# Performance work log

Hardware: AMD Instinct MI355X
Metric: run time of the kernel (lower is better)

Reference implementation:

```python
import jax, jax.numpy as jnp
import numpy as np
from jax import lax

T, H, K, V, O = 8192, 2048, 512, 512, 2048


def setup_inputs() -> dict:
    key = jax.random.key(0)
    ks = jax.random.split(key, 11)
    s_h = 1.0 / np.sqrt(H)
    s_v = 1.0 / np.sqrt(V)
    return {
        "hidden_state": jax.random.normal(ks[0], (T, H), jnp.float32),
        "Wq": jax.random.normal(ks[1], (H, K), jnp.float32) * s_h,
        "bq": jax.random.normal(ks[2], (K,), jnp.float32) * 0.02,
        "Wk": jax.random.normal(ks[3], (H, K), jnp.float32) * s_h,
        "bk": jax.random.normal(ks[4], (K,), jnp.float32) * 0.02,
        "Wv": jax.random.normal(ks[5], (H, V), jnp.float32) * s_h,
        "bv": jax.random.normal(ks[6], (V,), jnp.float32) * 0.02,
        "Wg": jax.random.normal(ks[7], (H, K), jnp.float32) * s_h,
        "bg": jax.random.normal(ks[8], (K,), jnp.float32) * 0.02,
        "Wo": jax.random.normal(ks[9], (V, O), jnp.float32) * s_v,
        "bo": jax.random.normal(ks[10], (O,), jnp.float32) * 0.02,
    }


def reference(hidden_state, Wq, bq, Wk, bk, Wv, bv, Wg, bg, Wo, bo):
    # Batched projections (torch Linear: x @ W^T + b; here W stored as [in,out])
    q = hidden_state @ Wq + bq                    # [T, K]
    k = jax.nn.sigmoid(hidden_state @ Wk + bk)    # [T, K]
    g = jax.nn.sigmoid(hidden_state @ Wg + bg)    # [T, K]
    v = hidden_state @ Wv + bv                    # [T, V]

    def step(state, qkvg):
        qi, ki, vi, gi = qkvg
        # state: [K, V]; gated decay per key-dim row, then outer-product write
        state = state * gi[:, None] + ki[:, None] * vi[None, :]
        out_i = qi @ state  # == state.T @ qi -> [V]
        return state, out_i

    init = jnp.zeros((K, V), hidden_state.dtype)
    final_state, outs = lax.scan(step, init, (q, k, v, g))  # outs: [T, V]
    output = outs @ Wo + bo                                  # [T, O]
    return output, final_state
```

## Files before the change

kernel.cpp:

```cpp
#include <hip/hip_runtime.h>

#define T_LEN 8192
#define H_DIM 2048
#define K_DIM 512
#define V_DIM 512
#define O_DIM 2048
#define CHUNK 64
#define NCHUNK 128

typedef short bf16x8 __attribute__((ext_vector_type(8)));
typedef float f32x4 __attribute__((ext_vector_type(4)));

typedef const __attribute__((address_space(1))) void* gptr1_t;
typedef __attribute__((address_space(3))) void* lptr3_t;

__device__ __forceinline__ float b2f(unsigned short u) {
    unsigned int i = ((unsigned int)u) << 16;
    float f;
    __builtin_memcpy(&f, &i, 4);
    return f;
}
__device__ __forceinline__ unsigned short f2b(float f) {
    unsigned int i;
    __builtin_memcpy(&i, &f, 4);
    unsigned int r = (i + 0x7FFFu + ((i >> 16) & 1u)) >> 16;
    return (unsigned short)r;
}
__device__ __forceinline__ float fw(float v) {
    return fminf(fmaxf(v, -1e30f), 1e30f);
}

#define BARX() asm volatile("s_barrier" ::: "memory")
#define ORDER() asm volatile("" ::: "memory")

#define GLDS(gp, dstByte)                                                      \
    __builtin_amdgcn_global_load_lds((gptr1_t)(const void*)(gp),               \
                                     (lptr3_t)(void*)((char*)lds + (dstByte)), \
                                     16, 0, 0)
#define STAGE2(p0, p1, dstBase)                                                \
    do {                                                                       \
        GLDS(p0, (dstBase) + tid * 16);                                        \
        GLDS(p1, (dstBase) + 8192 + tid * 16);                                 \
    } while (0)

__global__ __launch_bounds__(64) void probe_k(int* __restrict__ flag) {
    __shared__ unsigned short As[16 * 32];
    __shared__ unsigned short Bs[16 * 32];
    int tid = threadIdx.x;
    for (int idx = tid; idx < 512; idx += 64) {
        int r = idx >> 5, c = idx & 31;
        float av = (c == 0) ? (float)(r + 1) : (c == 1 ? 1.0f : 0.0f);
        float bv = (c == 0) ? 1.0f : (c == 1 ? (float)(1024 * (r + 1)) : 0.0f);
        As[r * 32 + c] = f2b(av);
        Bs[r * 32 + c] = f2b(bv);
    }
    __syncthreads();
    int ln15 = tid & 15, q4 = (tid & 63) >> 4;
    bf16x8 a = *(const bf16x8*)(As + ln15 * 32 + q4 * 8);
    bf16x8 b = *(const bf16x8*)(Bs + ln15 * 32 + q4 * 8);
    f32x4 acc = {0.f, 0.f, 0.f, 0.f};
    acc = __builtin_amdgcn_mfma_f32_16x16x32_bf16(a, b, acc, 0, 0, 0);
    bool h0 = true, h1 = true;
#pragma unroll
    for (int i = 0; i < 4; i++) {
        float e0 = (float)((q4 * 4 + i + 1) + 1024 * (ln15 + 1));
        float e1 = (float)((ln15 + 1) + 1024 * (q4 * 4 + i + 1));
        h0 = h0 && (acc[i] == e0);
        h1 = h1 && (acc[i] == e1);
    }
    unsigned long long b0 = __ballot(h0 ? 1 : 0);
    unsigned long long b1 = __ballot(h1 ? 1 : 0);
    if (tid == 0) *flag = (b0 == ~0ull) ? 0 : ((b1 == ~0ull) ? 1 : 0);
}

__global__ __launch_bounds__(256) void prep_k(const float* __restrict__ hs,
                                              unsigned short* __restrict__ hsb,
                                              const float* __restrict__ Wq,
                                              const float* __restrict__ Wk,
                                              const float* __restrict__ Wg,
                                              const float* __restrict__ Wv,
                                              const float* __restrict__ Wo,
                                              unsigned short* __restrict__ WT,
                                              unsigned short* __restrict__ WoT) {
    __shared__ unsigned short tile[32][33];
    long bid = blockIdx.x;
    int tid = threadIdx.x;
    if (bid < 8192) {
        long i = (bid * 256 + tid) * 8;
        unsigned int wd[4];
#pragma unroll
        for (int u = 0; u < 4; u++) {
            unsigned short lo = f2b(hs[i + 2 * u]);
            unsigned short hi = f2b(hs[i + 2 * u + 1]);
            wd[u] = (unsigned int)lo | ((unsigned int)hi << 16);
        }
        uint4 pk; pk.x = wd[0]; pk.y = wd[1]; pk.z = wd[2]; pk.w = wd[3];
        *(uint4*)(hsb + i) = pk;
        return;
    }
    int t = (int)(bid - 8192);
    int mat = t >> 10, tl = t & 1023;
    const float* in; unsigned short* outp; int R, C, br, bc;
    if (mat < 4) {
        in = mat == 0 ? Wq : mat == 1 ? Wk : mat == 2 ? Wg : Wv;
        outp = WT + (long)mat * 512 * H_DIM;
        R = H_DIM; C = 512; br = tl >> 4; bc = tl & 15;
    } else {
        in = Wo; outp = WoT; R = V_DIM; C = O_DIM; br = tl & 15; bc = tl >> 4;
    }
    int tc = tid & 31, tr = tid >> 5;
#pragma unroll
    for (int i = 0; i < 4; i++) {
        int r = tr + 8 * i;
        long idx = (long)(br * 32 + r) * C + bc * 32 + tc;
        tile[r][tc] = f2b(in[idx]);
    }
    __syncthreads();
#pragma unroll
    for (int i = 0; i < 4; i++) {
        int r = tr + 8 * i;
        outp[(long)(bc * 32 + r) * R + br * 32 + tc] = tile[tc][r];
    }
}

__global__ __launch_bounds__(512, 2) void proj_gemm256_k(const unsigned short* __restrict__ A,
                                                         const unsigned short* __restrict__ WT,
                                                         const float* __restrict__ bq,
                                                         const float* __restrict__ bk,
                                                         const float* __restrict__ bg,
                                                         const float* __restrict__ bv,
                                                         unsigned short* __restrict__ qb,
                                                         unsigned short* __restrict__ kb,
                                                         float* __restrict__ gb,
                                                         unsigned short* __restrict__ vT,
                                                         const int* __restrict__ flagp) {
    __shared__ short lds[65536];
    int fl = *flagp;
    int tid = threadIdx.x;
    int lane = tid & 63;
    int ln15 = lane & 15, q4 = lane >> 4;
    int w = tid >> 6;
    int wm = w >> 2, wn = w & 3;
    long m0 = (long)blockIdx.x * 256, n0 = (long)blockIdx.y * 256;

    unsigned slot = ((unsigned)(q4 * 16)) ^ ((unsigned)((ln15 & 7) << 4));
    unsigned aoff0 = (unsigned)(wm * 8192 + ln15 * 128) + slot;
    unsigned boff0 = 65536u + (unsigned)(wn * 4096 + ln15 * 128) + slot;

    int idx0 = tid, idx1 = 512 + tid;
    int r0_ = idx0 >> 3, r1_ = idx1 >> 3;
    int c80 = (idx0 & 7) ^ (r0_ & 7);
    int c81 = (idx1 & 7) ^ (r1_ & 7);
    int trA0 = ((r0_ >> 6) & 1) * 128 + (r0_ & 63);
    int trA1 = ((r1_ >> 6) & 1) * 128 + (r1_ & 63);
    int tcB0 = ((r0_ >> 5) & 3) * 64 + (r0_ & 31);
    int tcB1 = ((r1_ >> 5) & 3) * 64 + (r1_ & 31);
    const unsigned short* pAlo0 = A + (m0 + trA0) * (long)H_DIM + c80 * 8;
    const unsigned short* pAlo1 = A + (m0 + trA1) * (long)H_DIM + c81 * 8;
    const unsigned short* pAhi0 = pAlo0 + 64 * H_DIM;
    const unsigned short* pAhi1 = pAlo1 + 64 * H_DIM;
    const unsigned short* pBlo0 = WT + (n0 + tcB0) * (long)H_DIM + c80 * 8;
    const unsigned short* pBlo1 = WT + (n0 + tcB1) * (long)H_DIM + c81 * 8;
    const unsigned short* pBhi0 = pBlo0 + 32 * H_DIM;
    const unsigned short* pBhi1 = pBlo1 + 32 * H_DIM;

    f32x4 acc[8][4] = {};

    STAGE2(pAlo0, pAlo1, 0);
    STAGE2(pBlo0, pBlo1, 65536);
    ORDER();
    STAGE2(pBhi0, pBhi1, 65536 + 16384);
    STAGE2(pAhi0, pAhi1, 16384);
    ORDER();
    pAlo0 += 64; pAlo1 += 64; pBlo0 += 64; pBlo1 += 64;
    STAGE2(pAlo0, pAlo1, 32768);
    STAGE2(pBlo0, pBlo1, 65536 + 32768);
    ORDER();
    pAlo0 += 64; pAlo1 += 64; pBlo0 += 64; pBlo1 += 64;
    pAhi0 += 64; pAhi1 += 64; pBhi0 += 64; pBhi1 += 64;
    asm volatile("s_waitcnt vmcnt(8)" ::: "memory");
    BARX();

    int cur = 0;
    const char* L = (const char*)lds;
    for (int kt = 0; kt < H_DIM; kt += 64, cur ^= 1) {
        int nxt = cur ^ 1;
        unsigned bufb = (unsigned)cur << 15;
        unsigned ab0 = aoff0 + bufb, ab1 = ab0 ^ 64u;
        unsigned bb0 = boff0 + bufb, bb1 = bb0 ^ 64u;
        bf16x8 af[4][2], blo[2][2], bhi[2][2];

#pragma unroll
        for (int i = 0; i < 4; i++) {
            af[i][0] = *(const bf16x8*)(L + ab0 + i * 2048);
            af[i][1] = *(const bf16x8*)(L + ab1 + i * 2048);
        }
#pragma unroll
        for (int j = 0; j < 2; j++) {
            blo[j][0] = *(const bf16x8*)(L + bb0 + j * 2048);
            blo[j][1] = *(const bf16x8*)(L + bb1 + j * 2048);
        }
        STAGE2(pBhi0, pBhi1, 65536 + nxt * 32768 + 16384);
        BARX();
        __builtin_amdgcn_s_setprio(1);
#pragma unroll
        for (int i = 0; i < 4; i++)
#pragma unroll
            for (int j = 0; j < 2; j++) {
                acc[i][j] = __builtin_amdgcn_mfma_f32_16x16x32_bf16(af[i][0], blo[j][0], acc[i][j], 0, 0, 0);
                acc[i][j] = __builtin_amdgcn_mfma_f32_16x16x32_bf16(af[i][1], blo[j][1], acc[i][j], 0, 0, 0);
            }
        __builtin_amdgcn_s_setprio(0);
        asm volatile("s_waitcnt vmcnt(8)" ::: "memory");
        BARX();

#pragma unroll
        for (int j = 0; j < 2; j++) {
            bhi[j][0] = *(const bf16x8*)(L + bb0 + 16384 + j * 2048);
            bhi[j][1] = *(const bf16x8*)(L + bb1 + 16384 + j * 2048);
        }
        STAGE2(pAhi0, pAhi1, nxt * 32768 + 16384);
        BARX();
        __builtin_amdgcn_s_setprio(1);
#pragma unroll
        for (int i = 0; i < 4; i++)
#pragma unroll
            for (int j = 0; j < 2; j++) {
                acc[i][2 + j] = __builtin_amdgcn_mfma_f32_16x16x32_bf16(af[i][0], bhi[j][0], acc[i][2 + j], 0, 0, 0);
                acc[i][2 + j] = __builtin_amdgcn_mfma_f32_16x16x32_bf16(af[i][1], bhi[j][1], acc[i][2 + j], 0, 0, 0);
            }
        __builtin_amdgcn_s_setprio(0);
        asm volatile("s_waitcnt vmcnt(8)" ::: "memory");
        BARX();

#pragma unroll
        for (int i = 0; i < 4; i++) {
            af[i][0] = *(const bf16x8*)(L + ab0 + 16384 + i * 2048);
            af[i][1] = *(const bf16x8*)(L + ab1 + 16384 + i * 2048);
        }
        STAGE2(pAlo0, pAlo1, cur * 32768);
        BARX();
        __builtin_amdgcn_s_setprio(1);
#pragma unroll
        for (int i = 0; i < 4; i++)
#pragma unroll
            for (int j = 0; j < 2; j++) {
                acc[4 + i][2 + j] = __builtin_amdgcn_mfma_f32_16x16x32_bf16(af[i][0], bhi[j][0], acc[4 + i][2 + j], 0, 0, 0);
                acc[4 + i][2 + j] = __builtin_amdgcn_mfma_f32_16x16x32_bf16(af[i][1], bhi[j][1], acc[4 + i][2 + j], 0, 0, 0);
            }
        __builtin_amdgcn_s_setprio(0);
        BARX();

        STAGE2(pBlo0, pBlo1, 65536 + cur * 32768);
        __builtin_amdgcn_s_setprio(1);
#pragma unroll
        for (int i = 0; i < 4; i++)
#pragma unroll
            for (int j = 0; j < 2; j++) {
                acc[4 + i][j] = __builtin_amdgcn_mfma_f32_16x16x32_bf16(af[i][0], blo[j][0], acc[4 + i][j], 0, 0, 0);
                acc[4 + i][j] = __builtin_amdgcn_mfma_f32_16x16x32_bf16(af[i][1], blo[j][1], acc[4 + i][j], 0, 0, 0);
            }
        __builtin_amdgcn_s_setprio(0);
        asm volatile("s_waitcnt vmcnt(8)" ::: "memory");
        BARX();

        pAlo0 += 64; pAlo1 += 64; pAhi0 += 64; pAhi1 += 64;
        pBlo0 += 64; pBlo1 += 64; pBhi0 += 64; pBhi1 += 64;
    }

    int seg = (int)(n0 >> 9);
    int nl0 = (int)(n0 & 511);
    const float* bias = seg == 0 ? bq : seg == 1 ? bk : seg == 2 ? bg : bv;

    if (seg == 3 && fl == 0) {
#pragma unroll
        for (int im = 0; im < 8; im++)
#pragma unroll
            for (int jn = 0; jn < 4; jn++) {
                int nl = nl0 + wn * 64 + (jn >> 1) * 32 + (jn & 1) * 16 + ln15;
                float bsv = bias[nl];
                long mb = m0 + wm * 128 + (im >> 2) * 64 + (im & 3) * 16 + q4 * 4;
                unsigned short h0 = f2b(fw(acc[im][jn][0] + bsv));
                unsigned short h1 = f2b(fw(acc[im][jn][1] + bsv));
                unsigned short h2 = f2b(fw(acc[im][jn][2] + bsv));
                unsigned short h3 = f2b(fw(acc[im][jn][3] + bsv));
                uint2 pk;
                pk.x = (unsigned int)h0 | ((unsigned int)h1 << 16);
                pk.y = (unsigned int)h2 | ((unsigned int)h3 << 16);
                *(uint2*)(vT + (long)nl * T_LEN + mb) = pk;
            }
    } else {
#pragma unroll
        for (int im = 0; im < 8; im++)
#pragma unroll
            for (int jn = 0; jn < 4; jn++)
#pragma unroll
                for (int ii = 0; ii < 4; ii++) {
                    int dm = fl ? ln15 : q4 * 4 + ii;
                    int dn = fl ? q4 * 4 + ii : ln15;
                    long m = m0 + wm * 128 + (im >> 2) * 64 + (im & 3) * 16 + dm;
                    int nl = nl0 + wn * 64 + (jn >> 1) * 32 + (jn & 1) * 16 + dn;
                    float v = fw(acc[im][jn][ii] + bias[nl]);
                    if (seg == 1 || seg == 2) v = 1.0f / (1.0f + __expf(-v));
                    if (seg == 0)
                        qb[m * K_DIM + nl] = f2b(v);
                    else if (seg == 1)
                        kb[m * K_DIM + nl] = f2b(v);
                    else if (seg == 2)
                        gb[m * K_DIM + nl] = v;
                    else
                        vT[(long)nl * T_LEN + m] = f2b(v);
                }
    }
}

__global__ __launch_bounds__(512, 2) void gemm256_k(const unsigned short* __restrict__ A,
                                                    const unsigned short* __restrict__ BT,
                                                    const float* __restrict__ bias,
                                                    float* __restrict__ out,
                                                    int N, int KT,
                                                    const int* __restrict__ flagp) {
    __shared__ short lds[65536];
    int fl = *flagp;
    int tid = threadIdx.x;
    int lane = tid & 63;
    int ln15 = lane & 15, q4 = lane >> 4;
    int w = tid >> 6;
    int wm = w >> 2, wn = w & 3;
    long m0 = (long)blockIdx.x * 256, n0 = (long)blockIdx.y * 256;

    unsigned slot = ((unsigned)(q4 * 16)) ^ ((unsigned)((ln15 & 7) << 4));
    unsigned aoff0 = (unsigned)(wm * 8192 + ln15 * 128) + slot;
    unsigned boff0 = 65536u + (unsigned)(wn * 4096 + ln15 * 128) + slot;

    int idx0 = tid, idx1 = 512 + tid;
    int r0_ = idx0 >> 3, r1_ = idx1 >> 3;
    int c80 = (idx0 & 7) ^ (r0_ & 7);
    int c81 = (idx1 & 7) ^ (r1_ & 7);
    int trA0 = ((r0_ >> 6) & 1) * 128 + (r0_ & 63);
    int trA1 = ((r1_ >> 6) & 1) * 128 + (r1_ & 63);
    int tcB0 = ((r0_ >> 5) & 3) * 64 + (r0_ & 31);
    int tcB1 = ((r1_ >> 5) & 3) * 64 + (r1_ & 31);
    const unsigned short* pAlo0 = A + (m0 + trA0) * (long)KT + c80 * 8;
    const unsigned short* pAlo1 = A + (m0 + trA1) * (long)KT + c81 * 8;
    const unsigned short* pAhi0 = pAlo0 + 64 * KT;
    const unsigned short* pAhi1 = pAlo1 + 64 * KT;
    const unsigned short* pBlo0 = BT + (n0 + tcB0) * (long)KT + c80 * 8;
    const unsigned short* pBlo1 = BT + (n0 + tcB1) * (long)KT + c81 * 8;
    const unsigned short* pBhi0 = pBlo0 + 32 * KT;
    const unsigned short* pBhi1 = pBlo1 + 32 * KT;

    f32x4 acc[8][4] = {};

    STAGE2(pAlo0, pAlo1, 0);
    STAGE2(pBlo0, pBlo1, 65536);
    ORDER();
    STAGE2(pBhi0, pBhi1, 65536 + 16384);
    STAGE2(pAhi0, pAhi1, 16384);
    ORDER();
    pAlo0 += 64; pAlo1 += 64; pBlo0 += 64; pBlo1 += 64;
    STAGE2(pAlo0, pAlo1, 32768);
    STAGE2(pBlo0, pBlo1, 65536 + 32768);
    ORDER();
    pAlo0 += 64; pAlo1 += 64; pBlo0 += 64; pBlo1 += 64;
    pAhi0 += 64; pAhi1 += 64; pBhi0 += 64; pBhi1 += 64;
    asm volatile("s_waitcnt vmcnt(8)" ::: "memory");
    BARX();

    int cur = 0;
    const char* L = (const char*)lds;
    for (int kt = 0; kt < KT; kt += 64, cur ^= 1) {
        int nxt = cur ^ 1;
        unsigned bufb = (unsigned)cur << 15;
        unsigned ab0 = aoff0 + bufb, ab1 = ab0 ^ 64u;
        unsigned bb0 = boff0 + bufb, bb1 = bb0 ^ 64u;
        bf16x8 af[4][2], blo[2][2], bhi[2][2];

#pragma unroll
        for (int i = 0; i < 4; i++) {
            af[i][0] = *(const bf16x8*)(L + ab0 + i * 2048);
            af[i][1] = *(const bf16x8*)(L + ab1 + i * 2048);
        }
#pragma unroll
        for (int j = 0; j < 2; j++) {
            blo[j][0] = *(const bf16x8*)(L + bb0 + j * 2048);
            blo[j][1] = *(const bf16x8*)(L + bb1 + j * 2048);
        }
        STAGE2(pBhi0, pBhi1, 65536 + nxt * 32768 + 16384);
        BARX();
        __builtin_amdgcn_s_setprio(1);
#pragma unroll
        for (int i = 0; i < 4; i++)
#pragma unroll
            for (int j = 0; j < 2; j++) {
                acc[i][j] = __builtin_amdgcn_mfma_f32_16x16x32_bf16(af[i][0], blo[j][0], acc[i][j], 0, 0, 0);
                acc[i][j] = __builtin_amdgcn_mfma_f32_16x16x32_bf16(af[i][1], blo[j][1], acc[i][j], 0, 0, 0);
            }
        __builtin_amdgcn_s_setprio(0);
        asm volatile("s_waitcnt vmcnt(8)" ::: "memory");
        BARX();

#pragma unroll
        for (int j = 0; j < 2; j++) {
            bhi[j][0] = *(const bf16x8*)(L + bb0 + 16384 + j * 2048);
            bhi[j][1] = *(const bf16x8*)(L + bb1 + 16384 + j * 2048);
        }
        STAGE2(pAhi0, pAhi1, nxt * 32768 + 16384);
        BARX();
        __builtin_amdgcn_s_setprio(1);
#pragma unroll
        for (int i = 0; i < 4; i++)
#pragma unroll
            for (int j = 0; j < 2; j++) {
                acc[i][2 + j] = __builtin_amdgcn_mfma_f32_16x16x32_bf16(af[i][0], bhi[j][0], acc[i][2 + j], 0, 0, 0);
                acc[i][2 + j] = __builtin_amdgcn_mfma_f32_16x16x32_bf16(af[i][1], bhi[j][1], acc[i][2 + j], 0, 0, 0);
            }
        __builtin_amdgcn_s_setprio(0);
        asm volatile("s_waitcnt vmcnt(8)" ::: "memory");
        BARX();

#pragma unroll
        for (int i = 0; i < 4; i++) {
            af[i][0] = *(const bf16x8*)(L + ab0 + 16384 + i * 2048);
            af[i][1] = *(const bf16x8*)(L + ab1 + 16384 + i * 2048);
        }
        STAGE2(pAlo0, pAlo1, cur * 32768);
        BARX();
        __builtin_amdgcn_s_setprio(1);
#pragma unroll
        for (int i = 0; i < 4; i++)
#pragma unroll
            for (int j = 0; j < 2; j++) {
                acc[4 + i][2 + j] = __builtin_amdgcn_mfma_f32_16x16x32_bf16(af[i][0], bhi[j][0], acc[4 + i][2 + j], 0, 0, 0);
                acc[4 + i][2 + j] = __builtin_amdgcn_mfma_f32_16x16x32_bf16(af[i][1], bhi[j][1], acc[4 + i][2 + j], 0, 0, 0);
            }
        __builtin_amdgcn_s_setprio(0);
        BARX();

        STAGE2(pBlo0, pBlo1, 65536 + cur * 32768);
        __builtin_amdgcn_s_setprio(1);
#pragma unroll
        for (int i = 0; i < 4; i++)
#pragma unroll
            for (int j = 0; j < 2; j++) {
                acc[4 + i][j] = __builtin_amdgcn_mfma_f32_16x16x32_bf16(af[i][0], blo[j][0], acc[4 + i][j], 0, 0, 0);
                acc[4 + i][j] = __builtin_amdgcn_mfma_f32_16x16x32_bf16(af[i][1], blo[j][1], acc[4 + i][j], 0, 0, 0);
            }
        __builtin_amdgcn_s_setprio(0);
        asm volatile("s_waitcnt vmcnt(8)" ::: "memory");
        BARX();

        pAlo0 += 64; pAlo1 += 64; pAhi0 += 64; pAhi1 += 64;
        pBlo0 += 64; pBlo1 += 64; pBhi0 += 64; pBhi1 += 64;
    }

#pragma unroll
    for (int im = 0; im < 8; im++)
#pragma unroll
        for (int jn = 0; jn < 4; jn++)
#pragma unroll
            for (int ii = 0; ii < 4; ii++) {
                int dm = fl ? ln15 : q4 * 4 + ii;
                int dn = fl ? q4 * 4 + ii : ln15;
                long m = m0 + wm * 128 + (im >> 2) * 64 + (im & 3) * 16 + dm;
                long n = n0 + wn * 64 + (jn >> 1) * 32 + (jn & 1) * 16 + dn;
                out[m * N + n] = fw(acc[im][jn][ii] + bias[n]);
            }
}

__global__ __launch_bounds__(256) void cumprod_k(const float* __restrict__ g,
                                                 unsigned short* __restrict__ q,
                                                 unsigned short* __restrict__ k,
                                                 unsigned short* __restrict__ khatT,
                                                 float* __restrict__ pend) {
    __shared__ unsigned short tile[256][80];
    int c = blockIdx.x;
    int half = blockIdx.y;
    int tid = threadIdx.x;
    int d = half * 256 + tid;
    long base = (long)c * CHUNK * K_DIM + d;
    float gv[CHUNK];
#pragma unroll
    for (int s = 0; s < CHUNK; s++) gv[s] = g[base + (long)s * K_DIM];
    float P = 1.0f;
#pragma unroll
    for (int s = 0; s < CHUNK; s++) { P = fmaxf(P * gv[s], 1e-37f); gv[s] = P; }
    pend[c * K_DIM + d] = P;
    float Pend = P;
#pragma unroll
    for (int s8 = 0; s8 < CHUNK; s8 += 8) {
        unsigned int packed[4];
#pragma unroll
        for (int u = 0; u < 8; u++) {
            int s = s8 + u;
            long idx = base + (long)s * K_DIM;
            float Pc = gv[s];
            float qv = fw(b2f(q[idx]) * Pc);
            q[idx] = f2b(qv);
            float kv = b2f(k[idx]);
            float kt = kv / Pc;
            kt = fmaxf(fminf(kt, 3e37f), -3e37f);
            k[idx] = f2b(kt);
            float ratio = Pend / Pc;
            unsigned short kh = f2b(fw(kv * ratio));
            if (u & 1)
                packed[u >> 1] |= ((unsigned int)kh) << 16;
            else
                packed[u >> 1] = kh;
        }
        uint4 pk;
        pk.x = packed[0]; pk.y = packed[1]; pk.z = packed[2]; pk.w = packed[3];
        *(uint4*)&tile[tid][s8] = pk;
    }
    __syncthreads();
    int wv = tid >> 6, l = tid & 63;
    int colb = (l & 7) * 8;
#pragma unroll
    for (int j = 0; j < 8; j++) {
        int row = wv * 64 + j * 8 + (l >> 3);
        uint4 pk = *(const uint4*)&tile[row][colb];
        *(uint4*)(khatT + (long)(half * 256 + row) * T_LEN + c * CHUNK + colb) = pk;
    }
}

__global__ __launch_bounds__(256) void scan_k(const unsigned short* __restrict__ khatT,
                                              const unsigned short* __restrict__ vT,
                                              const float* __restrict__ pend,
                                              unsigned short* __restrict__ ST,
                                              float* __restrict__ fstate,
                                              const int* __restrict__ flagp) {
    int fl = *flagp;
    int lane = threadIdx.x & 63, w = threadIdx.x >> 6;
    int ln15 = lane & 15, q4 = lane >> 4;
    int k0 = (blockIdx.x & 15) * 32 + (w & 1) * 16;
    int v0 = (blockIdx.x >> 4) * 32 + (w >> 1) * 16;
    f32x4 acc = {0.f, 0.f, 0.f, 0.f};
    const unsigned short* kb_ = khatT + (long)(k0 + ln15) * T_LEN + q4 * 8;
    const unsigned short* vb_ = vT + (long)(v0 + ln15) * T_LEN + q4 * 8;

    bf16x8 kf0[2], vf0[2], kf1[2], vf1[2], kf2[2], vf2[2], kf3[2], vf3[2];
    float4 pdv[4];
    float pds[4];

#define LOADSET(s, c)                                                        \
    do {                                                                     \
        long off_ = (long)(c) * CHUNK;                                       \
        kf##s[0] = *(const bf16x8*)(kb_ + off_);                             \
        kf##s[1] = *(const bf16x8*)(kb_ + off_ + 32);                        \
        vf##s[0] = *(const bf16x8*)(vb_ + off_);                             \
        vf##s[1] = *(const bf16x8*)(vb_ + off_ + 32);                        \
        if (!fl)                                                             \
            pdv[s] = *(const float4*)(pend + (c) * K_DIM + k0 + q4 * 4);     \
        else                                                                 \
            pds[s] = pend[(c) * K_DIM + k0 + ln15];                          \
    } while (0)

    LOADSET(0, 0); LOADSET(1, 1); LOADSET(2, 2); LOADSET(3, 3);

#define STEP(s, c)                                                                             \
    do {                                                                                       \
        if (!fl) {                                                                             \
            uint2 pk_;                                                                         \
            pk_.x = (unsigned int)f2b(fw(acc[0])) | ((unsigned int)f2b(fw(acc[1])) << 16);     \
            pk_.y = (unsigned int)f2b(fw(acc[2])) | ((unsigned int)f2b(fw(acc[3])) << 16);     \
            *(uint2*)(ST + ((long)(c) * V_DIM + v0 + ln15) * K_DIM + k0 + q4 * 4) = pk_;       \
            acc[0] *= pdv[s].x; acc[1] *= pdv[s].y; acc[2] *= pdv[s].z; acc[3] *= pdv[s].w;    \
        } else {                                                                               \
            ST[((long)(c) * V_DIM + v0 + q4 * 4 + 0) * K_DIM + k0 + ln15] = f2b(fw(acc[0]));   \
            ST[((long)(c) * V_DIM + v0 + q4 * 4 + 1) * K_DIM + k0 + ln15] = f2b(fw(acc[1]));   \
            ST[((long)(c) * V_DIM + v0 + q4 * 4 + 2) * K_DIM + k0 + ln15] = f2b(fw(acc[2]));   \
            ST[((long)(c) * V_DIM + v0 + q4 * 4 + 3) * K_DIM + k0 + ln15] = f2b(fw(acc[3]));   \
            acc[0] *= pds[s]; acc[1] *= pds[s]; acc[2] *= pds[s]; acc[3] *= pds[s];            \
        }                                                                                      \
        acc = __builtin_amdgcn_mfma_f32_16x16x32_bf16(kf##s[0], vf##s[0], acc, 0, 0, 0);       \
        acc = __builtin_amdgcn_mfma_f32_16x16x32_bf16(kf##s[1], vf##s[1], acc, 0, 0, 0);       \
        int cp_ = (c) + 4;                                                                     \
        if (cp_ > NCHUNK - 1) cp_ = NCHUNK - 1;                                                \
        LOADSET(s, cp_);                                                                       \
    } while (0)

    for (int c = 0; c < NCHUNK; c += 4) {
        STEP(0, c);
        STEP(1, c + 1);
        STEP(2, c + 2);
        STEP(3, c + 3);
    }
#undef STEP
#undef LOADSET

#pragma unroll
    for (int i = 0; i < 4; i++) {
        int dk = fl ? ln15 : q4 * 4 + i;
        int dv = fl ? q4 * 4 + i : ln15;
        fstate[(long)(k0 + dk) * V_DIM + v0 + dv] = fw(acc[i]);
    }
}

__global__ __launch_bounds__(256) void intra_k(const unsigned short* __restrict__ qs,
                                               const unsigned short* __restrict__ ks,
                                               const unsigned short* __restrict__ vT,
                                               const unsigned short* __restrict__ ST,
                                               unsigned short* __restrict__ outs,
                                               const int* __restrict__ flagp) {
    __shared__ unsigned short Ab[64 * 72];
    int fl = *flagp;
    long cloc = blockIdx.x >> 1;
    int c = (int)cloc, h = blockIdx.x & 1;
    int lane = threadIdx.x & 63, w = threadIdx.x >> 6;
    int ln15 = lane & 15, q4 = lane >> 4;
    long t0 = (long)c * CHUNK;

    {
        f32x4 accA[4] = {};
        for (int kk = 0; kk < K_DIM; kk += 32) {
            bf16x8 a = *(const bf16x8*)(qs + (t0 + 16 * w + ln15) * K_DIM + kk + q4 * 8);
#pragma unroll
            for (int j = 0; j < 4; j++) {
                bf16x8 b = *(const bf16x8*)(ks + (t0 + 16 * j + ln15) * K_DIM + kk + q4 * 8);
                accA[j] = __builtin_amdgcn_mfma_f32_16x16x32_bf16(a, b, accA[j], 0, 0, 0);
            }
        }
#pragma unroll
        for (int j = 0; j < 4; j++)
#pragma unroll
            for (int i = 0; i < 4; i++) {
                int dt = fl ? ln15 : q4 * 4 + i;
                int ds = fl ? q4 * 4 + i : ln15;
                int tl = 16 * w + dt;
                int s = 16 * j + ds;
                float av = (s <= tl) ? accA[j][i] : 0.0f;
                Ab[tl * 72 + s] = f2b(fw(av));
            }
    }
    __syncthreads();

    int v0 = h * 256 + w * 64;
    f32x4 acc[4][4] = {};
    for (int kk = 0; kk < K_DIM; kk += 32) {
        bf16x8 a[4], b[4];
#pragma unroll
        for (int i = 0; i < 4; i++)
            a[i] = *(const bf16x8*)(qs + (t0 + 16 * i + ln15) * K_DIM + kk + q4 * 8);
#pragma unroll
        for (int j = 0; j < 4; j++)
            b[j] = *(const bf16x8*)(ST + (cloc * V_DIM + v0 + 16 * j + ln15) * K_DIM + kk + q4 * 8);
#pragma unroll
        for (int i = 0; i < 4; i++)
#pragma unroll
            for (int j = 0; j < 4; j++)
                acc[i][j] = __builtin_amdgcn_mfma_f32_16x16x32_bf16(a[i], b[j], acc[i][j], 0, 0, 0);
    }
#pragma unroll
    for (int s0 = 0; s0 < CHUNK; s0 += 32) {
        bf16x8 a[4], b[4];
#pragma unroll
        for (int i = 0; i < 4; i++)
            a[i] = *(const bf16x8*)(Ab + (16 * i + ln15) * 72 + s0 + q4 * 8);
#pragma unroll
        for (int j = 0; j < 4; j++)
            b[j] = *(const bf16x8*)(vT + (long)(v0 + 16 * j + ln15) * T_LEN + t0 + s0 + q4 * 8);
#pragma unroll
        for (int i = 0; i < 4; i++)
#pragma unroll
            for (int j = 0; j < 4; j++)
                acc[i][j] = __builtin_amdgcn_mfma_f32_16x16x32_bf16(a[i], b[j], acc[i][j], 0, 0, 0);
    }
#pragma unroll
    for (int i = 0; i < 4; i++)
#pragma unroll
        for (int j = 0; j < 4; j++)
#pragma unroll
            for (int ii = 0; ii < 4; ii++) {
                int dt = fl ? ln15 : q4 * 4 + ii;
                int dv = fl ? q4 * 4 + ii : ln15;
                outs[(t0 + 16 * i + dt) * V_DIM + v0 + 16 * j + dv] = f2b(fw(acc[i][j][ii]));
            }
}

extern "C" void kernel_launch(void* const* d_in, const int* in_sizes, int n_in,
                              void* d_out, int out_size, void* d_ws, size_t ws_size,
                              hipStream_t stream) {
    const float* hs = (const float*)d_in[0];
    const float* Wq = (const float*)d_in[1];
    const float* bq = (const float*)d_in[2];
    const float* Wk = (const float*)d_in[3];
    const float* bk = (const float*)d_in[4];
    const float* Wv = (const float*)d_in[5];
    const float* bv = (const float*)d_in[6];
    const float* Wg = (const float*)d_in[7];
    const float* bg = (const float*)d_in[8];
    const float* Wo = (const float*)d_in[9];
    const float* bo = (const float*)d_in[10];

    float* out = (float*)d_out;

    char* ws = (char*)d_ws;
    const size_t MB = 1024 * 1024;
    unsigned short* WT = (unsigned short*)(ws + 0 * MB);
    unsigned short* outsb = (unsigned short*)(ws + 0 * MB);
    unsigned short* WoT = (unsigned short*)(ws + 8 * MB);
    unsigned short* qb = (unsigned short*)(ws + 10 * MB);
    unsigned short* kb = (unsigned short*)(ws + 18 * MB);
    unsigned short* vTb = (unsigned short*)(ws + 26 * MB);
    unsigned short* khatT = (unsigned short*)(ws + 34 * MB);
    float* pend = (float*)(ws + 42 * MB);
    int* flags = (int*)(ws + 42 * MB + 256 * 1024);
    float* gb = (float*)(ws + 44 * MB);
    unsigned short* STb = (unsigned short*)(ws + 44 * MB);
    unsigned short* hsb = (unsigned short*)(ws + 60 * MB);
    float* fsspare = (float*)(ws + 108 * MB);
    (void)ws_size; (void)in_sizes; (void)n_in;

    float* finalst =
        ((long)out_size >= (long)T_LEN * O_DIM + (long)K_DIM * V_DIM)
            ? out + (long)T_LEN * O_DIM
            : fsspare;

    dim3 b256(256);
    hipMemsetAsync(flags, 0, 16, stream);
    probe_k<<<dim3(1), dim3(64), 0, stream>>>(flags);
    prep_k<<<dim3(8192 + 5 * 1024), b256, 0, stream>>>(hs, hsb, Wq, Wk, Wg, Wv, Wo, WT, WoT);
    proj_gemm256_k<<<dim3(T_LEN / 256, 8), dim3(512), 0, stream>>>(
        hsb, WT, bq, bk, bg, bv, qb, kb, gb, vTb, flags);
    cumprod_k<<<dim3(NCHUNK, K_DIM / 256), b256, 0, stream>>>(gb, qb, kb, khatT, pend);
    scan_k<<<dim3(256), b256, 0, stream>>>(khatT, vTb, pend, STb, finalst, flags);
    intra_k<<<dim3(2 * NCHUNK), b256, 0, stream>>>(qb, kb, vTb, STb, outsb, flags);
    gemm256_k<<<dim3(T_LEN / 256, O_DIM / 256), dim3(512), 0, stream>>>(
        outsb, WoT, bo, out, O_DIM, V_DIM, flags);
}
```

Before: 391.3 us.

## Fold MFMA layout probe into prep kernel, drop GEMM barriers, split intra_k finer

Moves the MFMA output-layout probe into an extra block of prep_k, removing a memset and a separate launch. It deletes several s_barrier instructions inside the two 256-tile GEMM main loops, relying on waitcnt plus the remaining barriers for ordering. It splits intra_k into four V-slices per chunk instead of two, doubling the grid and halving per-wave accumulators. Removing the barriers risks LDS races when buffers being staged are still being read by other waves.

Result: no change. 397.1 us (+1.5%).

```diff
diff --git a/kernel.cpp b/kernel.cpp
--- a/kernel.cpp
+++ b/kernel.cpp
@@ -43,36 +43,6 @@
         GLDS(p1, (dstBase) + 8192 + tid * 16);                                 \
     } while (0)
 
-__global__ __launch_bounds__(64) void probe_k(int* __restrict__ flag) {
-    __shared__ unsigned short As[16 * 32];
-    __shared__ unsigned short Bs[16 * 32];
-    int tid = threadIdx.x;
-    for (int idx = tid; idx < 512; idx += 64) {
-        int r = idx >> 5, c = idx & 31;
-        float av = (c == 0) ? (float)(r + 1) : (c == 1 ? 1.0f : 0.0f);
-        float bv = (c == 0) ? 1.0f : (c == 1 ? (float)(1024 * (r + 1)) : 0.0f);
-        As[r * 32 + c] = f2b(av);
-        Bs[r * 32 + c] = f2b(bv);
-    }
-    __syncthreads();
-    int ln15 = tid & 15, q4 = (tid & 63) >> 4;
-    bf16x8 a = *(const bf16x8*)(As + ln15 * 32 + q4 * 8);
-    bf16x8 b = *(const bf16x8*)(Bs + ln15 * 32 + q4 * 8);
-    f32x4 acc = {0.f, 0.f, 0.f, 0.f};
-    acc = __builtin_amdgcn_mfma_f32_16x16x32_bf16(a, b, acc, 0, 0, 0);
-    bool h0 = true, h1 = true;
-#pragma unroll
-    for (int i = 0; i < 4; i++) {
-        float e0 = (float)((q4 * 4 + i + 1) + 1024 * (ln15 + 1));
-        float e1 = (float)((ln15 + 1) + 1024 * (q4 * 4 + i + 1));
-        h0 = h0 && (acc[i] == e0);
-        h1 = h1 && (acc[i] == e1);
-    }
-    unsigned long long b0 = __ballot(h0 ? 1 : 0);
-    unsigned long long b1 = __ballot(h1 ? 1 : 0);
-    if (tid == 0) *flag = (b0 == ~0ull) ? 0 : ((b1 == ~0ull) ? 1 : 0);
-}
-
 __global__ __launch_bounds__(256) void prep_k(const float* __restrict__ hs,
                                               unsigned short* __restrict__ hsb,
                                               const float* __restrict__ Wq,
@@ -81,7 +51,8 @@
                                               const float* __restrict__ Wv,
                                               const float* __restrict__ Wo,
                                               unsigned short* __restrict__ WT,
-                                              unsigned short* __restrict__ WoT) {
+                                              unsigned short* __restrict__ WoT,
+                                              int* __restrict__ flag) {
     __shared__ unsigned short tile[32][33];
     long bid = blockIdx.x;
     int tid = threadIdx.x;
@@ -96,6 +67,37 @@
         }
         uint4 pk; pk.x = wd[0]; pk.y = wd[1]; pk.z = wd[2]; pk.w = wd[3];
         *(uint4*)(hsb + i) = pk;
+        return;
+    }
+    if (bid == 8192 + 5 * 1024) {
+        unsigned short* As = &tile[0][0];
+        unsigned short* Bs = &tile[0][0] + 512;
+        for (int idx = tid; idx < 512; idx += 256) {
+            int r = idx >> 5, c = idx & 31;
+            float av = (c == 0) ? (float)(r + 1) : (c == 1 ? 1.0f : 0.0f);
+            float bv = (c == 0) ? 1.0f : (c == 1 ? (float)(1024 * (r + 1)) : 0.0f);
+            As[idx] = f2b(av);
+            Bs[idx] = f2b(bv);
+        }
+        __syncthreads();
+        if (tid < 64) {
+            int ln15 = tid & 15, q4 = tid >> 4;
+            bf16x8 a = *(const bf16x8*)(As + ln15 * 32 + q4 * 8);
+            bf16x8 b = *(const bf16x8*)(Bs + ln15 * 32 + q4 * 8);
+            f32x4 acc = {0.f, 0.f, 0.f, 0.f};
+            acc = __builtin_amdgcn_mfma_f32_16x16x32_bf16(a, b, acc, 0, 0, 0);
+            bool h0 = true, h1 = true;
+#pragma unroll
+            for (int i = 0; i < 4; i++) {
+                float e0 = (float)((q4 * 4 + i + 1) + 1024 * (ln15 + 1));
+                float e1 = (float)((ln15 + 1) + 1024 * (q4 * 4 + i + 1));
+                h0 = h0 && (acc[i] == e0);
+                h1 = h1 && (acc[i] == e1);
+            }
+            unsigned long long b0 = __ballot(h0 ? 1 : 0);
+            unsigned long long b1 = __ballot(h1 ? 1 : 0);
+            if (tid == 0) *flag = (b0 == ~0ull) ? 0 : ((b1 == ~0ull) ? 1 : 0);
+        }
         return;
     }
     int t = (int)(bid - 8192);
@@ -201,7 +203,6 @@
             blo[j][1] = *(const bf16x8*)(L + bb1 + j * 2048);
         }
         STAGE2(pBhi0, pBhi1, 65536 + nxt * 32768 + 16384);
-        BARX();
         __builtin_amdgcn_s_setprio(1);
 #pragma unroll
         for (int i = 0; i < 4; i++)
@@ -220,7 +221,6 @@
             bhi[j][1] = *(const bf16x8*)(L + bb1 + 16384 + j * 2048);
         }
         STAGE2(pAhi0, pAhi1, nxt * 32768 + 16384);
-        BARX();
         __builtin_amdgcn_s_setprio(1);
 #pragma unroll
         for (int i = 0; i < 4; i++)
@@ -239,7 +239,6 @@
             af[i][1] = *(const bf16x8*)(L + ab1 + 16384 + i * 2048);
         }
         STAGE2(pAlo0, pAlo1, cur * 32768);
-        BARX();
         __builtin_amdgcn_s_setprio(1);
 #pragma unroll
         for (int i = 0; i < 4; i++)
@@ -249,7 +248,6 @@
                 acc[4 + i][2 + j] = __builtin_amdgcn_mfma_f32_16x16x32_bf16(af[i][1], bhi[j][1], acc[4 + i][2 + j], 0, 0, 0);
             }
         __builtin_amdgcn_s_setprio(0);
-        BARX();
 
         STAGE2(pBlo0, pBlo1, 65536 + cur * 32768);
         __builtin_amdgcn_s_setprio(1);
@@ -387,7 +385,6 @@
             blo[j][1] = *(const bf16x8*)(L + bb1 + j * 2048);
         }
         STAGE2(pBhi0, pBhi1, 65536 + nxt * 32768 + 16384);
-        BARX();
         __builtin_amdgcn_s_setprio(1);
 #pragma unroll
         for (int i = 0; i < 4; i++)
@@ -406,7 +403,6 @@
             bhi[j][1] = *(const bf16x8*)(L + bb1 + 16384 + j * 2048);
         }
         STAGE2(pAhi0, pAhi1, nxt * 32768 + 16384);
-        BARX();
         __builtin_amdgcn_s_setprio(1);
 #pragma unroll
         for (int i = 0; i < 4; i++)
@@ -425,7 +421,6 @@
             af[i][1] = *(const bf16x8*)(L + ab1 + 16384 + i * 2048);
         }
         STAGE2(pAlo0, pAlo1, cur * 32768);
-        BARX();
         __builtin_amdgcn_s_setprio(1);
 #pragma unroll
         for (int i = 0; i < 4; i++)
@@ -435,7 +430,6 @@
                 acc[4 + i][2 + j] = __builtin_amdgcn_mfma_f32_16x16x32_bf16(af[i][1], bhi[j][1], acc[4 + i][2 + j], 0, 0, 0);
             }
         __builtin_amdgcn_s_setprio(0);
-        BARX();
 
         STAGE2(pBlo0, pBlo1, 65536 + cur * 32768);
         __builtin_amdgcn_s_setprio(1);
@@ -604,8 +598,8 @@
                                                const int* __restrict__ flagp) {
     __shared__ unsigned short Ab[64 * 72];
     int fl = *flagp;
-    long cloc = blockIdx.x >> 1;
-    int c = (int)cloc, h = blockIdx.x & 1;
+    long cloc = blockIdx.x >> 2;
+    int c = (int)cloc, h = blockIdx.x & 3;
     int lane = threadIdx.x & 63, w = threadIdx.x >> 6;
     int ln15 = lane & 15, q4 = lane >> 4;
     long t0 = (long)c * CHUNK;
@@ -634,41 +628,41 @@
     }
     __syncthreads();
 
-    int v0 = h * 256 + w * 64;
-    f32x4 acc[4][4] = {};
+    int v0 = h * 128 + w * 32;
+    f32x4 acc[4][2] = {};
     for (int kk = 0; kk < K_DIM; kk += 32) {
-        bf16x8 a[4], b[4];
+        bf16x8 a[4], b[2];
 #pragma unroll
         for (int i = 0; i < 4; i++)
             a[i] = *(const bf16x8*)(qs + (t0 + 16 * i + ln15) * K_DIM + kk + q4 * 8);
 #pragma unroll
-        for (int j = 0; j < 4; j++)
+        for (int j = 0; j < 2; j++)
             b[j] = *(const bf16x8*)(ST + (cloc * V_DIM + v0 + 16 * j + ln15) * K_DIM + kk + q4 * 8);
 #pragma unroll
         for (int i = 0; i < 4; i++)
 #pragma unroll
-            for (int j = 0; j < 4; j++)
+            for (int j = 0; j < 2; j++)
                 acc[i][j] = __builtin_amdgcn_mfma_f32_16x16x32_bf16(a[i], b[j], acc[i][j], 0, 0, 0);
     }
 #pragma unroll
     for (int s0 = 0; s0 < CHUNK; s0 += 32) {
-        bf16x8 a[4], b[4];
+        bf16x8 a[4], b[2];
 #pragma unroll
         for (int i = 0; i < 4; i++)
             a[i] = *(const bf16x8*)(Ab + (16 * i + ln15) * 72 + s0 + q4 * 8);
 #pragma unroll
-        for (int j = 0; j < 4; j++)
+        for (int j = 0; j < 2; j++)
             b[j] = *(const bf16x8*)(vT + (long)(v0 + 16 * j + ln15) * T_LEN + t0 + s0 + q4 * 8);
 #pragma unroll
         for (int i = 0; i < 4; i++)
 #pragma unroll
-            for (int j = 0; j < 4; j++)
+            for (int j = 0; j < 2; j++)
                 acc[i][j] = __builtin_amdgcn_mfma_f32_16x16x32_bf16(a[i], b[j], acc[i][j], 0, 0, 0);
     }
 #pragma unroll
     for (int i = 0; i < 4; i++)
 #pragma unroll
-        for (int j = 0; j < 4; j++)
+        for (int j = 0; j < 2; j++)
 #pragma unroll
             for (int ii = 0; ii < 4; ii++) {
                 int dt = fl ? ln15 : q4 * 4 + ii;
@@ -717,14 +711,13 @@
             : fsspare;
 
     dim3 b256(256);
-    hipMemsetAsync(flags, 0, 16, stream);
-    probe_k<<<dim3(1), dim3(64), 0, stream>>>(flags);
-    prep_k<<<dim3(8192 + 5 * 1024), b256, 0, stream>>>(hs, hsb, Wq, Wk, Wg, Wv, Wo, WT, WoT);
+    prep_k<<<dim3(8192 + 5 * 1024 + 1), b256, 0, stream>>>(hs, hsb, Wq, Wk, Wg, Wv, Wo, WT, WoT,
+                                                           flags);
     proj_gemm256_k<<<dim3(T_LEN / 256, 8), dim3(512), 0, stream>>>(
         hsb, WT, bq, bk, bg, bv, qb, kb, gb, vTb, flags);
     cumprod_k<<<dim3(NCHUNK, K_DIM / 256), b256, 0, stream>>>(gb, qb, kb, khatT, pend);
     scan_k<<<dim3(256), b256, 0, stream>>>(khatT, vTb, pend, STb, finalst, flags);
-    intra_k<<<dim3(2 * NCHUNK), b256, 0, stream>>>(qb, kb, vTb, STb, outsb, flags);
+    intra_k<<<dim3(4 * NCHUNK), b256, 0, stream>>>(qb, kb, vTb, STb, outsb, flags);
     gemm256_k<<<dim3(T_LEN / 256, O_DIM / 256), dim3(512), 0, stream>>>(
         outsb, WoT, bo, out, O_DIM, V_DIM, flags);
 }
```
